# Optimization experiments

Hardware: AMD Instinct MI355X
Metric: run time of the kernel (lower is better)

The kernel has to match this reference:

```python
import jax, jax.numpy as jnp
import numpy as np

N, DEG, F, H, O, B = 100000, 16, 128, 128, 128, 8192


def setup_inputs() -> dict:
    key = jax.random.key(0)
    k1, k2, k3, k4, k5 = jax.random.split(key, 5)
    features = jax.random.normal(k1, (N, F), dtype=jnp.float32)
    w1 = jax.random.normal(k2, (2 * F, H), dtype=jnp.float32)
    w2 = jax.random.normal(k3, (2 * H, O), dtype=jnp.float32)
    neighbor_idx = jax.random.randint(k4, (N, DEG), 0, N, dtype=jnp.int32)
    nodes = jax.random.randint(k5, (B,), 0, N, dtype=jnp.int32)
    return {"features": features, "w1": w1, "w2": w2,
            "neighbor_idx": neighbor_idx, "nodes": nodes}


def reference(features, w1, w2, neighbor_idx, nodes):
    # Layer 1 (computed for all nodes, vectorized): mean-aggregate neighbor
    # raw features, concat with self features, project with w1.
    neigh_feat = features[neighbor_idx]                 # [N, DEG, F] gather
    agg1 = neigh_feat.mean(axis=1)                      # [N, F]
    h1 = jnp.concatenate([features, agg1], axis=-1) @ w1  # [N, H]

    # Layer 2 (batch nodes): mean-aggregate neighbor layer-1 embeddings,
    # concat with self layer-1 embedding, project with w2.
    h1_self = h1[nodes]                                 # [B, H]
    h1_neigh = h1[neighbor_idx[nodes]].mean(axis=1)     # [B, H]
    out = jnp.concatenate([h1_self, h1_neigh], axis=-1) @ w2  # [B, O]
    return out
```

## Files before the change

kernel.cpp:

```cpp
#include <hip/hip_runtime.h>


#define N_NODES 100000
#define DEG     16
#define FDIM    128
#define HDIM    128
#define B_NODES 8192

typedef __attribute__((ext_vector_type(8))) short bf16x8;
typedef __attribute__((ext_vector_type(8))) unsigned short u16x8;
typedef __attribute__((ext_vector_type(4))) float f32x4;
typedef __attribute__((ext_vector_type(2))) float f32x2;

static __device__ __forceinline__ unsigned short f2bf(float f) {
    union { float f; unsigned u; } v; v.f = f;
    unsigned r = v.u + 0x7fff + ((v.u >> 16) & 1);
    return (unsigned short)(r >> 16);
}
static __device__ __forceinline__ float bf2f(unsigned short b) {
    union { unsigned u; float f; } v; v.u = ((unsigned)b) << 16;
    return v.f;
}

__global__ __launch_bounds__(256)
void prep(const float* __restrict__ feat, const float* __restrict__ w1,
          const float* __restrict__ w2, unsigned char* __restrict__ f8,
          unsigned short* __restrict__ w1T, unsigned short* __restrict__ w2T) {
    if (blockIdx.x < 6250) {
        long e = ((long)blockIdx.x * 256 + threadIdx.x) * 8;
        float4 v0 = *(const float4*)(feat + e);
        float4 v1 = *(const float4*)(feat + e + 4);
        int p0 = 0, p1 = 0;
        p0 = __builtin_amdgcn_cvt_pk_fp8_f32(v0.x, v0.y, p0, false);
        p0 = __builtin_amdgcn_cvt_pk_fp8_f32(v0.z, v0.w, p0, true);
        p1 = __builtin_amdgcn_cvt_pk_fp8_f32(v1.x, v1.y, p1, false);
        p1 = __builtin_amdgcn_cvt_pk_fp8_f32(v1.z, v1.w, p1, true);
        uint2 o; o.x = (unsigned)p0; o.y = (unsigned)p1;
        *(uint2*)(f8 + e) = o;
    } else {
        int bid = blockIdx.x - 6250;
        const float* w = (bid < 8) ? w1 : w2;
        unsigned short* wT = (bid < 8) ? w1T : w2T;
        int kb = (bid & 7) * 32;
        int n = threadIdx.x & 127, dk = threadIdx.x >> 7;
#pragma unroll
        for (int i = 0; i < 16; ++i) {
            int k = kb + dk * 16 + i;
            wT[n * 256 + k] = f2bf(w[k * 128 + n]);
        }
    }
}

__global__ __launch_bounds__(256)
void k1_agg(const unsigned char* __restrict__ f8, const int* __restrict__ nbr,
            unsigned short* __restrict__ agg) {
    const int t = threadIdx.x;
    const int node = blockIdx.x * 16 + (t >> 4);
    const int cg = (t & 15) * 8;
    const int* idx = nbr + node * DEG;
    float s[8] = {0.f, 0.f, 0.f, 0.f, 0.f, 0.f, 0.f, 0.f};
#pragma unroll
    for (int d = 0; d < DEG; ++d) {
        int nb = idx[d];
        uint2 v = *(const uint2*)(f8 + (long)nb * FDIM + cg);
        f32x2 a0 = __builtin_amdgcn_cvt_pk_f32_fp8((int)v.x, false);
        f32x2 a1 = __builtin_amdgcn_cvt_pk_f32_fp8((int)v.x, true);
        f32x2 a2 = __builtin_amdgcn_cvt_pk_f32_fp8((int)v.y, false);
        f32x2 a3 = __builtin_amdgcn_cvt_pk_f32_fp8((int)v.y, true);
        s[0] += a0[0]; s[1] += a0[1]; s[2] += a1[0]; s[3] += a1[1];
        s[4] += a2[0]; s[5] += a2[1]; s[6] += a3[0]; s[7] += a3[1];
    }
    u16x8 o;
#pragma unroll
    for (int j = 0; j < 8; ++j) o[j] = f2bf(s[j] * 0.0625f);
    *(u16x8*)(agg + node * 128 + cg) = o;
}

__global__ __launch_bounds__(256)
void g1(const float* __restrict__ feat, const unsigned short* __restrict__ agg,
        const unsigned short* __restrict__ w1T, unsigned short* __restrict__ h1) {
    const int t = threadIdx.x, wave = t >> 6, lane = t & 63;
    const int m16 = lane & 15, quad = lane >> 4;
    const int row0 = blockIdx.x * 128;

    f32x4 acc[2][8] = {};
#pragma unroll
    for (int kc = 0; kc < 8; ++kc) {
        bf16x8 a[2], b[8];
#pragma unroll
        for (int mt = 0; mt < 2; ++mt) {
            int grow = row0 + wave * 32 + mt * 16 + m16;
            bf16x8 z = {};
            if (grow >= N_NODES) {
                a[mt] = z;
            } else if (kc < 4) {
                const float* p = feat + (long)grow * 128 + kc * 32 + quad * 8;
                float4 u0 = *(const float4*)p;
                float4 u1 = *(const float4*)(p + 4);
                bf16x8 c;
                c[0] = (short)f2bf(u0.x); c[1] = (short)f2bf(u0.y);
                c[2] = (short)f2bf(u0.z); c[3] = (short)f2bf(u0.w);
                c[4] = (short)f2bf(u1.x); c[5] = (short)f2bf(u1.y);
                c[6] = (short)f2bf(u1.z); c[7] = (short)f2bf(u1.w);
                a[mt] = c;
            } else {
                a[mt] = *(const bf16x8*)(agg + (long)grow * 128 + (kc - 4) * 32 + quad * 8);
            }
        }
#pragma unroll
        for (int nt = 0; nt < 8; ++nt)
            b[nt] = *(const bf16x8*)(w1T + (nt * 16 + m16) * 256 + kc * 32 + quad * 8);
#pragma unroll
        for (int mt = 0; mt < 2; ++mt)
#pragma unroll
            for (int nt = 0; nt < 8; ++nt)
                acc[mt][nt] = __builtin_amdgcn_mfma_f32_16x16x32_bf16(a[mt], b[nt], acc[mt][nt], 0, 0, 0);
    }

#pragma unroll
    for (int mt = 0; mt < 2; ++mt) {
        int rbase = row0 + wave * 32 + mt * 16 + quad * 4;
#pragma unroll
        for (int reg = 0; reg < 4; ++reg) {
            int grow = rbase + reg;
            if (grow >= N_NODES) continue;
#pragma unroll
            for (int nt = 0; nt < 8; ++nt)
                h1[grow * HDIM + nt * 16 + m16] = f2bf(acc[mt][nt][reg]);
        }
    }
}

__global__ __launch_bounds__(256)
void g2_fused(const unsigned short* __restrict__ h1, const unsigned short* __restrict__ w2T,
              const int* __restrict__ nbr, const int* __restrict__ nodes,
              float* __restrict__ out) {
    __shared__ unsigned short X2[64][264];
    const int t = threadIdx.x, wave = t >> 6, lane = t & 63;
    const int m16 = lane & 15, quad = lane >> 4;
    const int b0 = blockIdx.x * 64;
    const int colb = m16 * 8;

    for (int g = 0; g < 4; ++g) {
        int Ln = wave * 16 + g * 4 + quad;
        int node = nodes[b0 + Ln];
        *(u16x8*)(&X2[Ln][colb]) = *(const u16x8*)(h1 + node * HDIM + colb);
        const int* idx = nbr + node * DEG;
        float s[8] = {0.f, 0.f, 0.f, 0.f, 0.f, 0.f, 0.f, 0.f};
#pragma unroll
        for (int d = 0; d < DEG; ++d) {
            int nb = idx[d];
            u16x8 v = *(const u16x8*)(h1 + nb * HDIM + colb);
#pragma unroll
            for (int j = 0; j < 8; ++j) s[j] += bf2f(v[j]);
        }
        u16x8 o;
#pragma unroll
        for (int j = 0; j < 8; ++j) o[j] = f2bf(s[j] * 0.0625f);
        *(u16x8*)(&X2[Ln][128 + colb]) = o;
    }
    __syncthreads();

    f32x4 acc[8] = {};
#pragma unroll
    for (int kc = 0; kc < 8; ++kc) {
        bf16x8 a = *(const bf16x8*)(&X2[wave * 16 + m16][kc * 32 + quad * 8]);
#pragma unroll
        for (int nt = 0; nt < 8; ++nt) {
            bf16x8 b = *(const bf16x8*)(w2T + (nt * 16 + m16) * 256 + kc * 32 + quad * 8);
            acc[nt] = __builtin_amdgcn_mfma_f32_16x16x32_bf16(a, b, acc[nt], 0, 0, 0);
        }
    }

#pragma unroll
    for (int nt = 0; nt < 8; ++nt)
#pragma unroll
        for (int reg = 0; reg < 4; ++reg) {
            int row = b0 + wave * 16 + quad * 4 + reg;
            out[row * 128 + nt * 16 + m16] = acc[nt][reg];
        }
}

extern "C" void kernel_launch(void* const* d_in, const int* in_sizes, int n_in,
                              void* d_out, int out_size, void* d_ws, size_t ws_size,
                              hipStream_t stream) {
    const float* feat  = (const float*)d_in[0];
    const float* w1    = (const float*)d_in[1];
    const float* w2    = (const float*)d_in[2];
    const int*   nbr   = (const int*)d_in[3];
    const int*   nodes = (const int*)d_in[4];
    float* out = (float*)d_out;

    char* ws = (char*)d_ws;
    unsigned char*  f8  = (unsigned char*)ws;
    unsigned short* agg = (unsigned short*)(ws + 12800000);
    unsigned short* h1  = (unsigned short*)(ws + 38400000);
    unsigned short* w1T = (unsigned short*)(ws + 64000000);
    unsigned short* w2T = (unsigned short*)(ws + 64065536);

    prep<<<6266, 256, 0, stream>>>(feat, w1, w2, f8, w1T, w2T);
    k1_agg<<<6250, 256, 0, stream>>>(f8, nbr, agg);
    g1<<<(N_NODES + 127) / 128, 256, 0, stream>>>(feat, agg, w1T, h1);
    g2_fused<<<B_NODES / 64, 256, 0, stream>>>(h1, w2T, nbr, nodes, out);
}
```

Measured before the change: 185.6 us.

## Pre-convert features to bf16 and split g1 output columns across waves

```diff
diff --git a/kernel.cpp b/kernel.cpp
--- a/kernel.cpp
+++ b/kernel.cpp
@@ -24,19 +24,24 @@
 
 __global__ __launch_bounds__(256)
 void prep(const float* __restrict__ feat, const float* __restrict__ w1,
-          const float* __restrict__ w2, unsigned char* __restrict__ f8,
+          const float* __restrict__ w2, unsigned short* __restrict__ fb,
+          unsigned char* __restrict__ f8,
           unsigned short* __restrict__ w1T, unsigned short* __restrict__ w2T) {
     if (blockIdx.x < 6250) {
         long e = ((long)blockIdx.x * 256 + threadIdx.x) * 8;
         float4 v0 = *(const float4*)(feat + e);
         float4 v1 = *(const float4*)(feat + e + 4);
+        u16x8 ob;
+        ob[0] = f2bf(v0.x); ob[1] = f2bf(v0.y); ob[2] = f2bf(v0.z); ob[3] = f2bf(v0.w);
+        ob[4] = f2bf(v1.x); ob[5] = f2bf(v1.y); ob[6] = f2bf(v1.z); ob[7] = f2bf(v1.w);
+        *(u16x8*)(fb + e) = ob;
         int p0 = 0, p1 = 0;
         p0 = __builtin_amdgcn_cvt_pk_fp8_f32(v0.x, v0.y, p0, false);
         p0 = __builtin_amdgcn_cvt_pk_fp8_f32(v0.z, v0.w, p0, true);
         p1 = __builtin_amdgcn_cvt_pk_fp8_f32(v1.x, v1.y, p1, false);
         p1 = __builtin_amdgcn_cvt_pk_fp8_f32(v1.z, v1.w, p1, true);
-        uint2 o; o.x = (unsigned)p0; o.y = (unsigned)p1;
-        *(uint2*)(f8 + e) = o;
+        uint2 o8; o8.x = (unsigned)p0; o8.y = (unsigned)p1;
+        *(uint2*)(f8 + e) = o8;
     } else {
         int bid = blockIdx.x - 6250;
         const float* w = (bid < 8) ? w1 : w2;
@@ -76,58 +81,58 @@
     *(u16x8*)(agg + node * 128 + cg) = o;
 }
 
-__global__ __launch_bounds__(256)
-void g1(const float* __restrict__ feat, const unsigned short* __restrict__ agg,
+__global__ __launch_bounds__(256, 3)
+void g1(const unsigned short* __restrict__ fb, const unsigned short* __restrict__ agg,
         const unsigned short* __restrict__ w1T, unsigned short* __restrict__ h1) {
     const int t = threadIdx.x, wave = t >> 6, lane = t & 63;
     const int m16 = lane & 15, quad = lane >> 4;
     const int row0 = blockIdx.x * 128;
-
-    f32x4 acc[2][8] = {};
-#pragma unroll
-    for (int kc = 0; kc < 8; ++kc) {
-        bf16x8 a[2], b[8];
+    const int n0 = wave * 32;
+
+    bf16x8 B[8][2];
+#pragma unroll
+    for (int kc = 0; kc < 8; ++kc)
+#pragma unroll
+        for (int nt = 0; nt < 2; ++nt)
+            B[kc][nt] = *(const bf16x8*)(w1T + (n0 + nt * 16 + m16) * 256 + kc * 32 + quad * 8);
+
+    for (int c = 0; c < 4; ++c) {
+        const int r0 = row0 + c * 32;
+        bf16x8 A[2][8];
 #pragma unroll
         for (int mt = 0; mt < 2; ++mt) {
-            int grow = row0 + wave * 32 + mt * 16 + m16;
+            int grow = r0 + mt * 16 + m16;
+            bool ok = grow < N_NODES;
+            const unsigned short* pf = fb + (long)grow * 128 + quad * 8;
+            const unsigned short* pa = agg + (long)grow * 128 + quad * 8;
             bf16x8 z = {};
-            if (grow >= N_NODES) {
-                a[mt] = z;
-            } else if (kc < 4) {
-                const float* p = feat + (long)grow * 128 + kc * 32 + quad * 8;
-                float4 u0 = *(const float4*)p;
-                float4 u1 = *(const float4*)(p + 4);
-                bf16x8 c;
-                c[0] = (short)f2bf(u0.x); c[1] = (short)f2bf(u0.y);
-                c[2] = (short)f2bf(u0.z); c[3] = (short)f2bf(u0.w);
-                c[4] = (short)f2bf(u1.x); c[5] = (short)f2bf(u1.y);
-                c[6] = (short)f2bf(u1.z); c[7] = (short)f2bf(u1.w);
-                a[mt] = c;
-            } else {
-                a[mt] = *(const bf16x8*)(agg + (long)grow * 128 + (kc - 4) * 32 + quad * 8);
+#pragma unroll
+            for (int kc = 0; kc < 4; ++kc)
+                A[mt][kc] = ok ? *(const bf16x8*)(pf + kc * 32) : z;
+#pragma unroll
+            for (int kc = 4; kc < 8; ++kc)
+                A[mt][kc] = ok ? *(const bf16x8*)(pa + (kc - 4) * 32) : z;
+        }
+
+        f32x4 acc[2][2] = {};
+#pragma unroll
+        for (int kc = 0; kc < 8; ++kc)
+#pragma unroll
+            for (int mt = 0; mt < 2; ++mt)
+#pragma unroll
+                for (int nt = 0; nt < 2; ++nt)
+                    acc[mt][nt] = __builtin_amdgcn_mfma_f32_16x16x32_bf16(A[mt][kc], B[kc][nt], acc[mt][nt], 0, 0, 0);
+
+#pragma unroll
+        for (int mt = 0; mt < 2; ++mt)
+#pragma unroll
+            for (int reg = 0; reg < 4; ++reg) {
+                int grow = r0 + mt * 16 + quad * 4 + reg;
+                if (grow >= N_NODES) continue;
+#pragma unroll
+                for (int nt = 0; nt < 2; ++nt)
+                    h1[grow * HDIM + n0 + nt * 16 + m16] = f2bf(acc[mt][nt][reg]);
             }
-        }
-#pragma unroll
-        for (int nt = 0; nt < 8; ++nt)
-            b[nt] = *(const bf16x8*)(w1T + (nt * 16 + m16) * 256 + kc * 32 + quad * 8);
-#pragma unroll
-        for (int mt = 0; mt < 2; ++mt)
-#pragma unroll
-            for (int nt = 0; nt < 8; ++nt)
-                acc[mt][nt] = __builtin_amdgcn_mfma_f32_16x16x32_bf16(a[mt], b[nt], acc[mt][nt], 0, 0, 0);
-    }
-
-#pragma unroll
-    for (int mt = 0; mt < 2; ++mt) {
-        int rbase = row0 + wave * 32 + mt * 16 + quad * 4;
-#pragma unroll
-        for (int reg = 0; reg < 4; ++reg) {
-            int grow = rbase + reg;
-            if (grow >= N_NODES) continue;
-#pragma unroll
-            for (int nt = 0; nt < 8; ++nt)
-                h1[grow * HDIM + nt * 16 + m16] = f2bf(acc[mt][nt][reg]);
-        }
     }
 }
 
@@ -192,14 +197,15 @@
     float* out = (float*)d_out;
 
     char* ws = (char*)d_ws;
-    unsigned char*  f8  = (unsigned char*)ws;
-    unsigned short* agg = (unsigned short*)(ws + 12800000);
-    unsigned short* h1  = (unsigned short*)(ws + 38400000);
-    unsigned short* w1T = (unsigned short*)(ws + 64000000);
-    unsigned short* w2T = (unsigned short*)(ws + 64065536);
-
-    prep<<<6266, 256, 0, stream>>>(feat, w1, w2, f8, w1T, w2T);
+    unsigned short* fb  = (unsigned short*)ws;
+    unsigned char*  f8  = (unsigned char*)(ws + 25600000);
+    unsigned short* agg = (unsigned short*)(ws + 38400000);
+    unsigned short* h1  = (unsigned short*)(ws + 64000000);
+    unsigned short* w1T = (unsigned short*)(ws + 89600000);
+    unsigned short* w2T = (unsigned short*)(ws + 89665536);
+
+    prep<<<6266, 256, 0, stream>>>(feat, w1, w2, fb, f8, w1T, w2T);
     k1_agg<<<6250, 256, 0, stream>>>(f8, nbr, agg);
-    g1<<<(N_NODES + 127) / 128, 256, 0, stream>>>(feat, agg, w1T, h1);
+    g1<<<(N_NODES + 127) / 128, 256, 0, stream>>>(fb, agg, w1T, h1);
     g2_fused<<<B_NODES / 64, 256, 0, stream>>>(h1, w2T, nbr, nodes, out);
 }
```

Result: no change. 185.6 us (+0.0%).
